# Optimization experiments

Hardware: AMD Instinct MI355X
Metric: run time of the kernel (lower is better)

## Reference

```python
import jax, jax.numpy as jnp
import numpy as np

N = 20000   # nodes
E = 320000  # edges
G = 64      # graphs in batch
IN = 256    # in_dim
H = 256     # hidden_dim1
C = 2       # n_classes


def setup_inputs() -> dict:
    key = jax.random.key(0)
    ks = jax.random.split(key, 12)
    h = jax.random.normal(ks[0], (N, IN), jnp.float32)
    src = jax.random.randint(ks[1], (E,), 0, N)
    dst = jax.random.randint(ks[2], (E,), 0, N)
    graph_id = jnp.sort(jax.random.randint(ks[3], (N,), 0, G))
    s_in = 1.0 / np.sqrt(IN)
    s_h = 1.0 / np.sqrt(H)
    W_conv = jax.random.normal(ks[4], (IN, H), jnp.float32) * s_in
    b_conv = jnp.zeros((H,), jnp.float32)
    w_gate = jax.random.normal(ks[5], (H, 1), jnp.float32) * s_h
    b_gate = jnp.zeros((1,), jnp.float32)
    W1 = jax.random.normal(ks[6], (H, H), jnp.float32) * s_h
    b1 = jnp.zeros((H,), jnp.float32)
    W2 = jax.random.normal(ks[7], (H, C), jnp.float32) * s_h
    b2 = jnp.zeros((C,), jnp.float32)
    return dict(h=h, src=src, dst=dst, graph_id=graph_id, W_conv=W_conv,
                b_conv=b_conv, w_gate=w_gate, b_gate=b_gate, W1=W1, b1=b1,
                W2=W2, b2=b2)


def reference(h, src, dst, graph_id, W_conv, b_conv, w_gate, b_gate, W1, b1, W2, b2):
    ones_e = jnp.ones((E,), jnp.float32)
    # DGL GraphConv, norm='both': D_out^-1/2 on source, D_in^-1/2 on dest
    deg_out = jax.ops.segment_sum(ones_e, src, num_segments=N)
    deg_in = jax.ops.segment_sum(ones_e, dst, num_segments=N)
    hn = h * jax.lax.rsqrt(jnp.maximum(deg_out, 1.0))[:, None]
    hn = hn @ W_conv                       # [N, H] (weight applied before aggregation)
    agg = jax.ops.segment_sum(hn[src], dst, num_segments=N)  # gather + scatter-add
    agg = agg * jax.lax.rsqrt(jnp.maximum(deg_in, 1.0))[:, None] + b_conv
    hr = jax.nn.relu(agg)                  # F.relu after conv1
    # GlobalAttentionPooling: per-graph segment softmax over gate scores
    gate = hr @ w_gate + b_gate            # [N, 1]
    gmax = jax.ops.segment_max(gate, graph_id, num_segments=G)
    e = jnp.exp(gate - gmax[graph_id])
    denom = jax.ops.segment_sum(e, graph_id, num_segments=G)
    att = e / denom[graph_id]              # [N, 1] attention weights (g2)
    hg = jax.ops.segment_sum(att * hr, graph_id, num_segments=G)  # [G, H]
    # classifier heads (dropout is identity at inference)
    a2 = hg @ W1 + b1
    a3 = a2 @ W2 + b2
    return jax.nn.sigmoid(a3), att, hg
```

## Files before the change

### kernel.cpp

```cpp
#include <hip/hip_runtime.h>
#include <hip/hip_bf16.h>
#include <hip/hip_fp16.h>
#include <math.h>

#define NN 20000
#define EE 320000
#define GG 64
#define IND 256
#define HD 256
#define CC 2

typedef __hip_bfloat16 bf16;
typedef __attribute__((ext_vector_type(8))) short short8;
typedef __attribute__((ext_vector_type(4))) float f32x4;

__device__ __forceinline__ float b2f(bf16 x){ return __bfloat162float(x); }
__device__ __forceinline__ float bits2f(unsigned short b){
    union{ float f; unsigned u; } v; v.u = ((unsigned)b) << 16; return v.f;
}
__device__ __forceinline__ short f2bs(float x){
    union{ bf16 b; short s; } u; u.b = __float2bfloat16(x); return u.s;
}
__device__ __forceinline__ float ldf3(const void* p, size_t i, int c){
    if (c == 1) return b2f(((const bf16*)p)[i]);
    if (c == 2) return __half2float(((const __half*)p)[i]);
    return ((const float*)p)[i];
}
__device__ __forceinline__ int idec(const void* p, int i, int c){
    if (c == 1) return (int)(((const long long*)p)[i]);
    if (c == 2) return (int)(((const float*)p)[i]);
    if (c == 3) return (int)__half2float(((const __half*)p)[i]);
    return ((const int*)p)[i];
}
__device__ __forceinline__ int wdetect(const unsigned short* p){
    int cb = 0, cf = 0, nz = 0;
    for (int i = 0; i < 128; i += 2){
        unsigned u = p[i];
        nz += (u != 0);
        int e8 = (u >> 7) & 0xFF;
        int e5 = (u >> 10) & 0x1F;
        cb += (e8 >= 100 && e8 <= 141);
        cf += (e5 >= 4 && e5 <= 22);
    }
    return (nz < 8) ? 0 : (cb >= 60) ? 1 : ((cf >= 60) ? 2 : 0);
}

#define ZBLK 64
__global__ __launch_bounds__(256) void k_detect(const void* src, const void* dst,
                         const void* gid,
                         const unsigned short* h, const unsigned short* Wc,
                         const unsigned short* wg, const unsigned short* W1,
                         const unsigned short* W2, const unsigned short* bc,
                         int* icode, int* dcode, int* zero_base,
                         bf16* __restrict__ Wb){
    int blk = blockIdx.x;
    if (blk < 3){
        if (threadIdx.x != 0) return;
        const void* buf = (blk == 0) ? src : (blk == 1) ? dst : gid;
        int n     = (blk == 2) ? NN : EE;
        int bound = (blk == 2) ? GG : NN;
        int ok64 = 1, ok32 = 1, okf32 = 1, okf16 = 1;
        const long long* p64 = (const long long*)buf;
        for (int i = 0; i < 64; i++){
            long long v = p64[n/8 + i];
            if (v < 0 || v >= (long long)bound) ok64 = 0;
        }
        const int* p32 = (const int*)buf;
        const unsigned* pu = (const unsigned*)buf;
        for (int i = 0; i < 64; i++){
            int v = p32[n/4 + i];
            if (v < 0 || v >= bound) ok32 = 0;
            float f = __uint_as_float(pu[n/4 + i]);
            if (!(f >= 0.f && f < (float)bound)) okf32 = 0;
        }
        const __half* ph = (const __half*)buf;
        for (int i = 0; i < 64; i++){
            float f = __half2float(ph[n/2 + i]);
            if (!(f >= 0.f && f < (float)bound)) okf16 = 0;
        }
        icode[blk] = ok64 ? 1 : (ok32 ? 0 : (okf32 ? 2 : (okf16 ? 3 : 0)));
    } else if (blk == 3){
        int t = threadIdx.x; if (t >= 6) return;
        const unsigned short* p = t==0?h:t==1?Wc:t==2?wg:t==3?W1:t==4?W2:bc;
        dcode[t] = wdetect(p);
    } else if (blk < 4 + IND){
        int k = blk - 4;
        __shared__ int code;
        if (threadIdx.x == 0) code = wdetect(Wc);
        __syncthreads();
        int c = code;
        int n = threadIdx.x;
        Wb[(size_t)n*IND + k] = __float2bfloat16(ldf3(Wc, (size_t)k*HD + n, c));
    } else {
        int idx = (blk - (4 + IND))*256 + threadIdx.x;
        const int total = 3*NN + GG*HD;
        for (int i = idx; i < total; i += ZBLK*256) zero_base[i] = 0;
    }
}

__global__ void k_prep(const void* src_r, const void* dst_r, const void* gid_r,
                       const int* __restrict__ icode,
                       int* __restrict__ gid_i,
                       int* cnt_out, int* cnt_in){
    int i = blockIdx.x*256 + threadIdx.x;
    if (i < NN) gid_i[i] = idec(gid_r, i, icode[2]);
    if (i >= EE) return;
    int s = idec(src_r, i, icode[0]);
    int d = idec(dst_r, i, icode[1]);
    if ((unsigned)s < NN) atomicAdd(&cnt_out[s], 1);
    if ((unsigned)d < NN) atomicAdd(&cnt_in[d], 1);
}

__global__ __launch_bounds__(1024) void k_scan(const int* __restrict__ cnt_out,
                                               const int* __restrict__ cnt_in,
                                               const int* __restrict__ gid,
                                               float* rs_out, float* rs_in,
                                               int* __restrict__ row_start,
                                               int* gstart, int* gend){
    int t = threadIdx.x;
    for (int i = t; i < NN; i += 1024){
        rs_out[i] = rsqrtf(fmaxf((float)cnt_out[i], 1.f));
        rs_in[i]  = rsqrtf(fmaxf((float)cnt_in[i], 1.f));
    }
    __shared__ int part[1024];
    const int per = (NN + 1023)/1024;
    int lo = t*per, hi = min(lo+per, NN);
    int s = 0;
    for (int i = lo; i < hi; i++) s += cnt_in[i];
    part[t] = s; __syncthreads();
    for (int off = 1; off < 1024; off <<= 1){
        int v = (t >= off) ? part[t-off] : 0;
        __syncthreads();
        part[t] += v;
        __syncthreads();
    }
    int base = part[t] - s;
    for (int i = lo; i < hi; i++){ row_start[i] = base; base += cnt_in[i]; }
    if (t == 1023) row_start[NN] = part[1023];
    __shared__ int ls[GG+1];
    if (t <= GG){
        int a = 0, b = NN;
        while (a < b){
            int mid = (a + b) >> 1;
            if (gid[mid] < t) a = mid + 1; else b = mid;
        }
        ls[t] = a;
    }
    __syncthreads();
    if (t < GG){ gstart[t] = ls[t]; gend[t] = ls[t+1]; }
}

#define GEMMB (NN/32)
#define FILLB ((EE+255)/256)
__global__ __launch_bounds__(256) void k_fillgemm(const void* __restrict__ h,
                                                  const bf16* __restrict__ Wb,
                                                  const float* __restrict__ rs_out,
                                                  const void* __restrict__ src_r,
                                                  const void* __restrict__ dst_r,
                                                  const int* __restrict__ icode,
                                                  const int* __restrict__ dcode,
                                                  const int* __restrict__ row_start,
                                                  int* __restrict__ cursor,
                                                  int* __restrict__ csr_src,
                                                  bf16* __restrict__ hn){
    int blk = blockIdx.x;
    if (blk >= GEMMB){
        int e = (blk - GEMMB)*256 + threadIdx.x;
        if (e >= EE) return;
        int s = idec(src_r, e, icode[0]);
        int d = idec(dst_r, e, icode[1]);
        if ((unsigned)s >= NN || (unsigned)d >= NN) return;
        int pos = atomicAdd(&cursor[d], 1);
        csr_src[row_start[d] + pos] = s;
        return;
    }
    int fh = dcode[0];
    int tid = threadIdx.x;
    int wave = tid >> 6, lane = tid & 63;
    int q = lane >> 4, mr = lane & 15;
    int row0 = blk * 32;
    int ncol0 = wave * 64;
    f32x4 acc[2][4] = {};
    const float* hf = (const float*)h;
    #pragma unroll
    for (int k0 = 0; k0 < IND; k0 += 32){
        short8 a[2], b[4];
        if (fh == 0){
            #pragma unroll
            for (int mi = 0; mi < 2; mi++){
                int r = row0 + mi*16 + mr;
                const float4* p = (const float4*)(hf + (size_t)r*IND + k0 + q*8);
                float4 v0 = p[0], v1 = p[1];
                a[mi][0] = f2bs(v0.x); a[mi][1] = f2bs(v0.y);
                a[mi][2] = f2bs(v0.z); a[mi][3] = f2bs(v0.w);
                a[mi][4] = f2bs(v1.x); a[mi][5] = f2bs(v1.y);
                a[mi][6] = f2bs(v1.z); a[mi][7] = f2bs(v1.w);
            }
        } else {
            #pragma unroll
            for (int mi = 0; mi < 2; mi++){
                int r = row0 + mi*16 + mr;
                #pragma unroll
                for (int j = 0; j < 8; j++)
                    a[mi][j] = f2bs(ldf3(h, (size_t)r*IND + k0 + q*8 + j, fh));
            }
        }
        #pragma unroll
        for (int ni = 0; ni < 4; ni++)
            b[ni] = *reinterpret_cast<const short8*>(
                        Wb + (size_t)(ncol0 + ni*16 + mr)*IND + k0 + q*8);
        #pragma unroll
        for (int mi = 0; mi < 2; mi++)
            #pragma unroll
            for (int ni = 0; ni < 4; ni++)
                acc[mi][ni] = __builtin_amdgcn_mfma_f32_16x16x32_bf16(
                                  a[mi], b[ni], acc[mi][ni], 0, 0, 0);
    }
    #pragma unroll
    for (int mi = 0; mi < 2; mi++){
        int rowb = row0 + mi*16 + q*4;
        #pragma unroll
        for (int r = 0; r < 4; r++){
            int row = rowb + r;
            float rs = rs_out[row];
            #pragma unroll
            for (int ni = 0; ni < 4; ni++)
                hn[(size_t)row*HD + ncol0 + ni*16 + mr] =
                    __float2bfloat16(acc[mi][ni][r] * rs);
        }
    }
}

__global__ __launch_bounds__(256) void k_gather(const bf16* __restrict__ hn,
                                                const float* __restrict__ rs_in,
                                                const int* __restrict__ row_start,
                                                const int* __restrict__ csr_src,
                                                const void* __restrict__ b_conv,
                                                const void* __restrict__ w_gate,
                                                const void* __restrict__ b_gate,
                                                const int* __restrict__ dcode,
                                                float* __restrict__ hr,
                                                float* __restrict__ gate){
    int wave = threadIdx.x >> 6, lane = threadIdx.x & 63;
    int n = blockIdx.x*4 + wave;
    if (n >= NN) return;
    int lo = row_start[n], hi = row_start[n+1];
    int half = lane >> 5, l2 = lane & 31;
    float a0=0.f,a1=0.f,a2=0.f,a3=0.f,a4=0.f,a5=0.f,a6=0.f,a7=0.f;
    int j = lo;
    for (; j + 8 <= hi; j += 8){
        int sA = csr_src[j+0+half], sB = csr_src[j+2+half];
        int sC = csr_src[j+4+half], sD = csr_src[j+6+half];
        short8 uA = *reinterpret_cast<const short8*>(hn + (size_t)sA*HD + l2*8);
        short8 uB = *reinterpret_cast<const short8*>(hn + (size_t)sB*HD + l2*8);
        short8 uC = *reinterpret_cast<const short8*>(hn + (size_t)sC*HD + l2*8);
        short8 uD = *reinterpret_cast<const short8*>(hn + (size_t)sD*HD + l2*8);
        a0 += bits2f((unsigned short)uA[0]) + bits2f((unsigned short)uB[0])
            + bits2f((unsigned short)uC[0]) + bits2f((unsigned short)uD[0]);
        a1 += bits2f((unsigned short)uA[1]) + bits2f((unsigned short)uB[1])
            + bits2f((unsigned short)uC[1]) + bits2f((unsigned short)uD[1]);
        a2 += bits2f((unsigned short)uA[2]) + bits2f((unsigned short)uB[2])
            + bits2f((unsigned short)uC[2]) + bits2f((unsigned short)uD[2]);
        a3 += bits2f((unsigned short)uA[3]) + bits2f((unsigned short)uB[3])
            + bits2f((unsigned short)uC[3]) + bits2f((unsigned short)uD[3]);
        a4 += bits2f((unsigned short)uA[4]) + bits2f((unsigned short)uB[4])
            + bits2f((unsigned short)uC[4]) + bits2f((unsigned short)uD[4]);
        a5 += bits2f((unsigned short)uA[5]) + bits2f((unsigned short)uB[5])
            + bits2f((unsigned short)uC[5]) + bits2f((unsigned short)uD[5]);
        a6 += bits2f((unsigned short)uA[6]) + bits2f((unsigned short)uB[6])
            + bits2f((unsigned short)uC[6]) + bits2f((unsigned short)uD[6]);
        a7 += bits2f((unsigned short)uA[7]) + bits2f((unsigned short)uB[7])
            + bits2f((unsigned short)uC[7]) + bits2f((unsigned short)uD[7]);
    }
    for (; j + 2 <= hi; j += 2){
        int s = csr_src[j+half];
        short8 u = *reinterpret_cast<const short8*>(hn + (size_t)s*HD + l2*8);
        a0 += bits2f((unsigned short)u[0]); a1 += bits2f((unsigned short)u[1]);
        a2 += bits2f((unsigned short)u[2]); a3 += bits2f((unsigned short)u[3]);
        a4 += bits2f((unsigned short)u[4]); a5 += bits2f((unsigned short)u[5]);
        a6 += bits2f((unsigned short)u[6]); a7 += bits2f((unsigned short)u[7]);
    }
    if (j < hi && half == 0){
        int s = csr_src[j];
        short8 u = *reinterpret_cast<const short8*>(hn + (size_t)s*HD + l2*8);
        a0 += bits2f((unsigned short)u[0]); a1 += bits2f((unsigned short)u[1]);
        a2 += bits2f((unsigned short)u[2]); a3 += bits2f((unsigned short)u[3]);
        a4 += bits2f((unsigned short)u[4]); a5 += bits2f((unsigned short)u[5]);
        a6 += bits2f((unsigned short)u[6]); a7 += bits2f((unsigned short)u[7]);
    }
    float send0 = half ? a0 : a4;
    float send1 = half ? a1 : a5;
    float send2 = half ? a2 : a6;
    float send3 = half ? a3 : a7;
    float recv0 = __shfl_xor(send0, 32);
    float recv1 = __shfl_xor(send1, 32);
    float recv2 = __shfl_xor(send2, 32);
    float recv3 = __shfl_xor(send3, 32);
    float tot0 = (half ? a4 : a0) + recv0;
    float tot1 = (half ? a5 : a1) + recv1;
    float tot2 = (half ? a6 : a2) + recv2;
    float tot3 = (half ? a7 : a3) + recv3;
    int db = dcode[5], fg = dcode[2];
    float rsn = rs_in[n];
    int c = l2*8 + half*4;
    float v0 = fmaxf(fmaf(tot0, rsn, ldf3(b_conv, c+0, db)), 0.f);
    float v1 = fmaxf(fmaf(tot1, rsn, ldf3(b_conv, c+1, db)), 0.f);
    float v2 = fmaxf(fmaf(tot2, rsn, ldf3(b_conv, c+2, db)), 0.f);
    float v3 = fmaxf(fmaf(tot3, rsn, ldf3(b_conv, c+3, db)), 0.f);
    float4 fv; fv.x = v0; fv.y = v1; fv.z = v2; fv.w = v3;
    *(float4*)(hr + (size_t)n*HD + c) = fv;
    float g = v0*ldf3(w_gate, c+0, fg) + v1*ldf3(w_gate, c+1, fg)
            + v2*ldf3(w_gate, c+2, fg) + v3*ldf3(w_gate, c+3, fg);
    #pragma unroll
    for (int off = 32; off; off >>= 1) g += __shfl_down(g, off);
    if (lane == 0) gate[n] = g + ldf3(b_gate, 0, db);
}

__global__ __launch_bounds__(256) void k_softhg(const float* __restrict__ gate,
                                                const float* __restrict__ hr,
                                                const int* __restrict__ gstart,
                                                const int* __restrict__ gend,
                                                float* __restrict__ hg,
                                                float* __restrict__ out_att){
    int g = blockIdx.x >> 3, part = blockIdx.x & 7;
    int t = threadIdx.x, lane = t & 63, wid = t >> 6;
    int lo = gstart[g], hi = gend[g], len = hi - lo;
    if (len <= 0) return;
    __shared__ float red[4];
    float m = -INFINITY;
    for (int n = lo + t; n < hi; n += 256) m = fmaxf(m, gate[n]);
    #pragma unroll
    for (int off = 32; off; off >>= 1) m = fmaxf(m, __shfl_xor(m, off));
    if (lane == 0) red[wid] = m;
    __syncthreads();
    m = fmaxf(fmaxf(red[0], red[1]), fmaxf(red[2], red[3]));
    __syncthreads();
    float s = 0.f;
    for (int n = lo + t; n < hi; n += 256) s += expf(gate[n] - m);
    #pragma unroll
    for (int off = 32; off; off >>= 1) s += __shfl_xor(s, off);
    if (lane == 0) red[wid] = s;
    __syncthreads();
    s = red[0] + red[1] + red[2] + red[3];
    float inv = 1.f / s;
    int chunk = (len + 7) >> 3;
    int plo = lo + part*chunk, phi = min(plo + chunk, hi);
    if (plo >= phi) return;
    for (int n = plo + t; n < phi; n += 256)
        out_att[n] = expf(gate[n] - m) * inv;
    float a0 = 0.f, a1 = 0.f, a2 = 0.f, a3 = 0.f;
    int r = plo;
    for (; r + 4 <= phi; r += 4){
        float w0 = expf(gate[r+0] - m) * inv;
        float w1 = expf(gate[r+1] - m) * inv;
        float w2 = expf(gate[r+2] - m) * inv;
        float w3 = expf(gate[r+3] - m) * inv;
        a0 = fmaf(w0, hr[(size_t)(r+0)*HD + t], a0);
        a1 = fmaf(w1, hr[(size_t)(r+1)*HD + t], a1);
        a2 = fmaf(w2, hr[(size_t)(r+2)*HD + t], a2);
        a3 = fmaf(w3, hr[(size_t)(r+3)*HD + t], a3);
    }
    for (; r < phi; r++)
        a0 = fmaf(expf(gate[r] - m) * inv, hr[(size_t)r*HD + t], a0);
    atomicAdd(&hg[g*HD + t], (a0 + a1) + (a2 + a3));
}

__global__ __launch_bounds__(256) void k_cls(const float* __restrict__ hg,
                                             const void* __restrict__ W1,
                                             const void* __restrict__ b1,
                                             const void* __restrict__ W2,
                                             const void* __restrict__ b2,
                                             const int* __restrict__ dcode,
                                             float* __restrict__ out0,
                                             float* __restrict__ out_hg){
    int f1 = dcode[3], f2 = dcode[4], db = dcode[5];
    int g = blockIdx.x, tid = threadIdx.x;
    __shared__ float hs[256];
    float hv = hg[g*HD + tid];
    hs[tid] = hv;
    out_hg[g*HD + tid] = hv;
    __syncthreads();
    float acc = ldf3(b1, tid, db);
    if (f1 == 1){
        const bf16* w = (const bf16*)W1;
        for (int k = 0; k < HD; k++) acc += hs[k]*b2f(w[(size_t)k*HD + tid]);
    } else if (f1 == 2){
        const __half* w = (const __half*)W1;
        for (int k = 0; k < HD; k++) acc += hs[k]*__half2float(w[(size_t)k*HD + tid]);
    } else {
        const float* w = (const float*)W1;
        for (int k = 0; k < HD; k++) acc += hs[k]*w[(size_t)k*HD + tid];
    }
    float p0 = acc * ldf3(W2, tid*CC + 0, f2);
    float p1 = acc * ldf3(W2, tid*CC + 1, f2);
    __shared__ float r0[256], r1[256];
    r0[tid] = p0; r1[tid] = p1; __syncthreads();
    for (int s = 128; s; s >>= 1){
        if (tid < s){ r0[tid] += r0[tid+s]; r1[tid] += r1[tid+s]; }
        __syncthreads();
    }
    if (tid == 0){
        out0[g*CC+0] = 1.f/(1.f + expf(-(r0[0] + ldf3(b2, 0, db))));
        out0[g*CC+1] = 1.f/(1.f + expf(-(r1[0] + ldf3(b2, 1, db))));
    }
}

extern "C" void kernel_launch(void* const* d_in, const int* in_sizes, int n_in,
                              void* d_out, int out_size, void* d_ws, size_t ws_size,
                              hipStream_t stream) {
    const void* h      = d_in[0];
    const void* src_r  = d_in[1];
    const void* dst_r  = d_in[2];
    const void* gid_r  = d_in[3];
    const void* W_conv = d_in[4];
    const void* b_conv = d_in[5];
    const void* w_gate = d_in[6];
    const void* b_gate = d_in[7];
    const void* W1     = d_in[8];
    const void* b1     = d_in[9];
    const void* W2     = d_in[10];
    const void* b2     = d_in[11];

    float* out     = (float*)d_out;
    float* out0    = out;
    float* out_att = out + GG*CC;
    float* out_hg  = out + GG*CC + NN;

    char* w = (char*)d_ws;
    float* hr   = (float*)w;  w += (size_t)NN*HD*sizeof(float);
    bf16*  hn   = (bf16*)w;   w += (size_t)NN*HD*sizeof(bf16);
    bf16*  Wb   = (bf16*)w;   w += (size_t)IND*HD*sizeof(bf16);
    float* rs_o = (float*)w;  w += (size_t)NN*sizeof(float);
    float* rs_i = (float*)w;  w += (size_t)NN*sizeof(float);
    float* gate = (float*)w;  w += (size_t)NN*sizeof(float);
    int* gstart = (int*)w;    w += GG*sizeof(int);
    int* gend   = (int*)w;    w += GG*sizeof(int);
    int* dcode  = (int*)w;    w += 8*sizeof(int);
    int* icode  = (int*)w;    w += 8*sizeof(int);
    int* gid_i  = (int*)w;    w += (size_t)NN*sizeof(int);
    int* cnt_out= (int*)w;    w += (size_t)NN*sizeof(int);
    int* cnt_in = (int*)w;    w += (size_t)NN*sizeof(int);
    int* cursor = (int*)w;    w += (size_t)NN*sizeof(int);
    float* hg   = (float*)w;  w += (size_t)GG*HD*sizeof(float);
    int* rowst  = (int*)w;    w += (size_t)(NN+1)*sizeof(int);
    int* csr    = (int*)w;    w += (size_t)EE*sizeof(int);

    k_detect<<<4 + IND + ZBLK, 256, 0, stream>>>(src_r, dst_r, gid_r,
                                     (const unsigned short*)h, (const unsigned short*)W_conv,
                                     (const unsigned short*)w_gate, (const unsigned short*)W1,
                                     (const unsigned short*)W2, (const unsigned short*)b_conv,
                                     icode, dcode, cnt_out, Wb);

    k_prep<<<(EE+255)/256, 256, 0, stream>>>(src_r, dst_r, gid_r, icode,
                                             gid_i, cnt_out, cnt_in);
    k_scan<<<1, 1024, 0, stream>>>(cnt_out, cnt_in, gid_i, rs_o, rs_i,
                                   rowst, gstart, gend);

    k_fillgemm<<<GEMMB + FILLB, 256, 0, stream>>>(h, Wb, rs_o, src_r, dst_r,
                                                  icode, dcode, rowst, cursor,
                                                  csr, hn);

    k_gather<<<(NN+3)/4, 256, 0, stream>>>(hn, rs_i, rowst, csr,
                                           b_conv, w_gate, b_gate, dcode, hr, gate);

    k_softhg<<<GG*8, 256, 0, stream>>>(gate, hr, gstart, gend, hg, out_att);

    k_cls<<<GG, 256, 0, stream>>>(hg, W1, b1, W2, b2, dcode, out0, out_hg);
}
```

Measured before the change: 234.7 us.

## Move source-degree scaling into gather and overlap GEMM with degree counting

```diff
diff --git a/kernel.cpp b/kernel.cpp
--- a/kernel.cpp
+++ b/kernel.cpp
@@ -32,20 +32,18 @@
     if (c == 3) return (int)__half2float(((const __half*)p)[i]);
     return ((const int*)p)[i];
 }
-__device__ __forceinline__ int wdetect(const unsigned short* p){
-    int cb = 0, cf = 0, nz = 0;
-    for (int i = 0; i < 128; i += 2){
-        unsigned u = p[i];
-        nz += (u != 0);
-        int e8 = (u >> 7) & 0xFF;
-        int e5 = (u >> 10) & 0x1F;
-        cb += (e8 >= 100 && e8 <= 141);
-        cf += (e5 >= 4 && e5 <= 22);
-    }
+__device__ __forceinline__ int wdetect_wave(const unsigned short* p, int t){
+    unsigned u = p[2*t];
+    int e8 = (u >> 7) & 0xFF;
+    int e5 = (u >> 10) & 0x1F;
+    int nz = __popcll(__ballot(u != 0));
+    int cb = __popcll(__ballot(e8 >= 100 && e8 <= 141));
+    int cf = __popcll(__ballot(e5 >= 4 && e5 <= 22));
     return (nz < 8) ? 0 : (cb >= 60) ? 1 : ((cf >= 60) ? 2 : 0);
 }
 
 #define ZBLK 64
+#define DETB (9 + IND)
 __global__ __launch_bounds__(256) void k_detect(const void* src, const void* dst,
                          const void* gid,
                          const unsigned short* h, const unsigned short* Wc,
@@ -54,124 +52,67 @@
                          int* icode, int* dcode, int* zero_base,
                          bf16* __restrict__ Wb){
     int blk = blockIdx.x;
+    int t = threadIdx.x;
     if (blk < 3){
-        if (threadIdx.x != 0) return;
+        if (t >= 64) return;
         const void* buf = (blk == 0) ? src : (blk == 1) ? dst : gid;
         int n     = (blk == 2) ? NN : EE;
         int bound = (blk == 2) ? GG : NN;
-        int ok64 = 1, ok32 = 1, okf32 = 1, okf16 = 1;
-        const long long* p64 = (const long long*)buf;
-        for (int i = 0; i < 64; i++){
-            long long v = p64[n/8 + i];
-            if (v < 0 || v >= (long long)bound) ok64 = 0;
+        long long v64 = ((const long long*)buf)[n/8 + t];
+        unsigned long long bad64 = __ballot(v64 < 0 || v64 >= (long long)bound);
+        int v32 = ((const int*)buf)[n/4 + t];
+        unsigned long long bad32 = __ballot(v32 < 0 || v32 >= bound);
+        float f32v = __uint_as_float(((const unsigned*)buf)[n/4 + t]);
+        unsigned long long badf32 = __ballot(!(f32v >= 0.f && f32v < (float)bound));
+        float f16v = __half2float(((const __half*)buf)[n/2 + t]);
+        unsigned long long badf16 = __ballot(!(f16v >= 0.f && f16v < (float)bound));
+        if (t == 0)
+            icode[blk] = (bad64 == 0ull) ? 1 : ((bad32 == 0ull) ? 0 :
+                         ((badf32 == 0ull) ? 2 : ((badf16 == 0ull) ? 3 : 0)));
+    } else if (blk < 9){
+        if (t >= 64) return;
+        int b = blk - 3;
+        const unsigned short* p = b==0?h:b==1?Wc:b==2?wg:b==3?W1:b==4?W2:bc;
+        int code = wdetect_wave(p, t);
+        if (t == 0) dcode[b] = code;
+    } else if (blk < DETB){
+        int k = blk - 9;
+        __shared__ int scode;
+        if (t < 64){
+            int code = wdetect_wave(Wc, t);
+            if (t == 0) scode = code;
         }
-        const int* p32 = (const int*)buf;
-        const unsigned* pu = (const unsigned*)buf;
-        for (int i = 0; i < 64; i++){
-            int v = p32[n/4 + i];
-            if (v < 0 || v >= bound) ok32 = 0;
-            float f = __uint_as_float(pu[n/4 + i]);
-            if (!(f >= 0.f && f < (float)bound)) okf32 = 0;
-        }
-        const __half* ph = (const __half*)buf;
-        for (int i = 0; i < 64; i++){
-            float f = __half2float(ph[n/2 + i]);
-            if (!(f >= 0.f && f < (float)bound)) okf16 = 0;
-        }
-        icode[blk] = ok64 ? 1 : (ok32 ? 0 : (okf32 ? 2 : (okf16 ? 3 : 0)));
-    } else if (blk == 3){
-        int t = threadIdx.x; if (t >= 6) return;
-        const unsigned short* p = t==0?h:t==1?Wc:t==2?wg:t==3?W1:t==4?W2:bc;
-        dcode[t] = wdetect(p);
-    } else if (blk < 4 + IND){
-        int k = blk - 4;
-        __shared__ int code;
-        if (threadIdx.x == 0) code = wdetect(Wc);
         __syncthreads();
-        int c = code;
-        int n = threadIdx.x;
-        Wb[(size_t)n*IND + k] = __float2bfloat16(ldf3(Wc, (size_t)k*HD + n, c));
+        int c = scode;
+        Wb[(size_t)t*IND + k] = __float2bfloat16(ldf3(Wc, (size_t)k*HD + t, c));
     } else {
-        int idx = (blk - (4 + IND))*256 + threadIdx.x;
+        int idx = (blk - DETB)*256 + t;
         const int total = 3*NN + GG*HD;
         for (int i = idx; i < total; i += ZBLK*256) zero_base[i] = 0;
     }
 }
 
-__global__ void k_prep(const void* src_r, const void* dst_r, const void* gid_r,
-                       const int* __restrict__ icode,
-                       int* __restrict__ gid_i,
-                       int* cnt_out, int* cnt_in){
-    int i = blockIdx.x*256 + threadIdx.x;
-    if (i < NN) gid_i[i] = idec(gid_r, i, icode[2]);
-    if (i >= EE) return;
-    int s = idec(src_r, i, icode[0]);
-    int d = idec(dst_r, i, icode[1]);
-    if ((unsigned)s < NN) atomicAdd(&cnt_out[s], 1);
-    if ((unsigned)d < NN) atomicAdd(&cnt_in[d], 1);
-}
-
-__global__ __launch_bounds__(1024) void k_scan(const int* __restrict__ cnt_out,
-                                               const int* __restrict__ cnt_in,
-                                               const int* __restrict__ gid,
-                                               float* rs_out, float* rs_in,
-                                               int* __restrict__ row_start,
-                                               int* gstart, int* gend){
-    int t = threadIdx.x;
-    for (int i = t; i < NN; i += 1024){
-        rs_out[i] = rsqrtf(fmaxf((float)cnt_out[i], 1.f));
-        rs_in[i]  = rsqrtf(fmaxf((float)cnt_in[i], 1.f));
-    }
-    __shared__ int part[1024];
-    const int per = (NN + 1023)/1024;
-    int lo = t*per, hi = min(lo+per, NN);
-    int s = 0;
-    for (int i = lo; i < hi; i++) s += cnt_in[i];
-    part[t] = s; __syncthreads();
-    for (int off = 1; off < 1024; off <<= 1){
-        int v = (t >= off) ? part[t-off] : 0;
-        __syncthreads();
-        part[t] += v;
-        __syncthreads();
-    }
-    int base = part[t] - s;
-    for (int i = lo; i < hi; i++){ row_start[i] = base; base += cnt_in[i]; }
-    if (t == 1023) row_start[NN] = part[1023];
-    __shared__ int ls[GG+1];
-    if (t <= GG){
-        int a = 0, b = NN;
-        while (a < b){
-            int mid = (a + b) >> 1;
-            if (gid[mid] < t) a = mid + 1; else b = mid;
-        }
-        ls[t] = a;
-    }
-    __syncthreads();
-    if (t < GG){ gstart[t] = ls[t]; gend[t] = ls[t+1]; }
-}
-
 #define GEMMB (NN/32)
-#define FILLB ((EE+255)/256)
-__global__ __launch_bounds__(256) void k_fillgemm(const void* __restrict__ h,
+#define PREPB ((EE+255)/256)
+__global__ __launch_bounds__(256) void k_prepgemm(const void* __restrict__ h,
                                                   const bf16* __restrict__ Wb,
-                                                  const float* __restrict__ rs_out,
                                                   const void* __restrict__ src_r,
                                                   const void* __restrict__ dst_r,
+                                                  const void* __restrict__ gid_r,
                                                   const int* __restrict__ icode,
                                                   const int* __restrict__ dcode,
-                                                  const int* __restrict__ row_start,
-                                                  int* __restrict__ cursor,
-                                                  int* __restrict__ csr_src,
+                                                  int* __restrict__ gid_i,
+                                                  int* cnt_out, int* cnt_in,
                                                   bf16* __restrict__ hn){
     int blk = blockIdx.x;
     if (blk >= GEMMB){
-        int e = (blk - GEMMB)*256 + threadIdx.x;
-        if (e >= EE) return;
-        int s = idec(src_r, e, icode[0]);
-        int d = idec(dst_r, e, icode[1]);
-        if ((unsigned)s >= NN || (unsigned)d >= NN) return;
-        int pos = atomicAdd(&cursor[d], 1);
-        csr_src[row_start[d] + pos] = s;
+        int i = (blk - GEMMB)*256 + threadIdx.x;
+        if (i < NN) gid_i[i] = idec(gid_r, i, icode[2]);
+        if (i >= EE) return;
+        int s = idec(src_r, i, icode[0]);
+        int d = idec(dst_r, i, icode[1]);
+        if ((unsigned)s < NN) atomicAdd(&cnt_out[s], 1);
+        if ((unsigned)d < NN) atomicAdd(&cnt_in[d], 1);
         return;
     }
     int fh = dcode[0];
@@ -222,16 +163,68 @@
         #pragma unroll
         for (int r = 0; r < 4; r++){
             int row = rowb + r;
-            float rs = rs_out[row];
             #pragma unroll
             for (int ni = 0; ni < 4; ni++)
                 hn[(size_t)row*HD + ncol0 + ni*16 + mr] =
-                    __float2bfloat16(acc[mi][ni][r] * rs);
+                    __float2bfloat16(acc[mi][ni][r]);
         }
     }
 }
 
+__global__ __launch_bounds__(1024) void k_scan(const int* __restrict__ cnt_out,
+                                               const int* __restrict__ cnt_in,
+                                               const int* __restrict__ gid,
+                                               float* rs_out, float* rs_in,
+                                               int* __restrict__ row_start,
+                                               int* gstart, int* gend){
+    int t = threadIdx.x;
+    for (int i = t; i < NN; i += 1024){
+        rs_out[i] = rsqrtf(fmaxf((float)cnt_out[i], 1.f));
+        rs_in[i]  = rsqrtf(fmaxf((float)cnt_in[i], 1.f));
+    }
+    __shared__ int part[1024];
+    const int per = (NN + 1023)/1024;
+    int lo = t*per, hi = min(lo+per, NN);
+    int s = 0;
+    for (int i = lo; i < hi; i++) s += cnt_in[i];
+    part[t] = s; __syncthreads();
+    for (int off = 1; off < 1024; off <<= 1){
+        int v = (t >= off) ? part[t-off] : 0;
+        __syncthreads();
+        part[t] += v;
+        __syncthreads();
+    }
+    int base = part[t] - s;
+    for (int i = lo; i < hi; i++){ row_start[i] = base; base += cnt_in[i]; }
+    if (t == 1023) row_start[NN] = part[1023];
+    __shared__ int ls[GG+1];
+    if (t <= GG){
+        int a = 0, b = NN;
+        while (a < b){
+            int mid = (a + b) >> 1;
+            if (gid[mid] < t) a = mid + 1; else b = mid;
+        }
+        ls[t] = a;
+    }
+    __syncthreads();
+    if (t < GG){ gstart[t] = ls[t]; gend[t] = ls[t+1]; }
+}
+
+__global__ void k_fill(const void* src_r, const void* dst_r,
+                       const int* __restrict__ icode,
+                       const int* __restrict__ row_start, int* __restrict__ cursor,
+                       int* __restrict__ csr_src){
+    int e = blockIdx.x*256 + threadIdx.x;
+    if (e >= EE) return;
+    int s = idec(src_r, e, icode[0]);
+    int d = idec(dst_r, e, icode[1]);
+    if ((unsigned)s >= NN || (unsigned)d >= NN) return;
+    int pos = atomicAdd(&cursor[d], 1);
+    csr_src[row_start[d] + pos] = s;
+}
+
 __global__ __launch_bounds__(256) void k_gather(const bf16* __restrict__ hn,
+                                                const float* __restrict__ rs_out,
                                                 const float* __restrict__ rs_in,
                                                 const int* __restrict__ row_start,
                                                 const int* __restrict__ csr_src,
@@ -251,42 +244,69 @@
     for (; j + 8 <= hi; j += 8){
         int sA = csr_src[j+0+half], sB = csr_src[j+2+half];
         int sC = csr_src[j+4+half], sD = csr_src[j+6+half];
+        float rA = rs_out[sA], rB = rs_out[sB], rC = rs_out[sC], rD = rs_out[sD];
         short8 uA = *reinterpret_cast<const short8*>(hn + (size_t)sA*HD + l2*8);
         short8 uB = *reinterpret_cast<const short8*>(hn + (size_t)sB*HD + l2*8);
         short8 uC = *reinterpret_cast<const short8*>(hn + (size_t)sC*HD + l2*8);
         short8 uD = *reinterpret_cast<const short8*>(hn + (size_t)sD*HD + l2*8);
-        a0 += bits2f((unsigned short)uA[0]) + bits2f((unsigned short)uB[0])
-            + bits2f((unsigned short)uC[0]) + bits2f((unsigned short)uD[0]);
-        a1 += bits2f((unsigned short)uA[1]) + bits2f((unsigned short)uB[1])
-            + bits2f((unsigned short)uC[1]) + bits2f((unsigned short)uD[1]);
-        a2 += bits2f((unsigned short)uA[2]) + bits2f((unsigned short)uB[2])
-            + bits2f((unsigned short)uC[2]) + bits2f((unsigned short)uD[2]);
-        a3 += bits2f((unsigned short)uA[3]) + bits2f((unsigned short)uB[3])
-            + bits2f((unsigned short)uC[3]) + bits2f((unsigned short)uD[3]);
-        a4 += bits2f((unsigned short)uA[4]) + bits2f((unsigned short)uB[4])
-            + bits2f((unsigned short)uC[4]) + bits2f((unsigned short)uD[4]);
-        a5 += bits2f((unsigned short)uA[5]) + bits2f((unsigned short)uB[5])
-            + bits2f((unsigned short)uC[5]) + bits2f((unsigned short)uD[5]);
-        a6 += bits2f((unsigned short)uA[6]) + bits2f((unsigned short)uB[6])
-            + bits2f((unsigned short)uC[6]) + bits2f((unsigned short)uD[6]);
-        a7 += bits2f((unsigned short)uA[7]) + bits2f((unsigned short)uB[7])
-            + bits2f((unsigned short)uC[7]) + bits2f((unsigned short)uD[7]);
+        a0 = fmaf(rA, bits2f((unsigned short)uA[0]),
+             fmaf(rB, bits2f((unsigned short)uB[0]),
+             fmaf(rC, bits2f((unsigned short)uC[0]),
+             fmaf(rD, bits2f((unsigned short)uD[0]), a0))));
+        a1 = fmaf(rA, bits2f((unsigned short)uA[1]),
+             fmaf(rB, bits2f((unsigned short)uB[1]),
+             fmaf(rC, bits2f((unsigned short)uC[1]),
+             fmaf(rD, bits2f((unsigned short)uD[1]), a1))));
+        a2 = fmaf(rA, bits2f((unsigned short)uA[2]),
+             fmaf(rB, bits2f((unsigned short)uB[2]),
+             fmaf(rC, bits2f((unsigned short)uC[2]),
+             fmaf(rD, bits2f((unsigned short)uD[2]), a2))));
+        a3 = fmaf(rA, bits2f((unsigned short)uA[3]),
+             fmaf(rB, bits2f((unsigned short)uB[3]),
+             fmaf(rC, bits2f((unsigned short)uC[3]),
+             fmaf(rD, bits2f((unsigned short)uD[3]), a3))));
+        a4 = fmaf(rA, bits2f((unsigned short)uA[4]),
+             fmaf(rB, bits2f((unsigned short)uB[4]),
+             fmaf(rC, bits2f((unsigned short)uC[4]),
+             fmaf(rD, bits2f((unsigned short)uD[4]), a4))));
+        a5 = fmaf(rA, bits2f((unsigned short)uA[5]),
+             fmaf(rB, bits2f((unsigned short)uB[5]),
+             fmaf(rC, bits2f((unsigned short)uC[5]),
+             fmaf(rD, bits2f((unsigned short)uD[5]), a5))));
+        a6 = fmaf(rA, bits2f((unsigned short)uA[6]),
+             fmaf(rB, bits2f((unsigned short)uB[6]),
+             fmaf(rC, bits2f((unsigned short)uC[6]),
+             fmaf(rD, bits2f((unsigned short)uD[6]), a6))));
+        a7 = fmaf(rA, bits2f((unsigned short)uA[7]),
+             fmaf(rB, bits2f((unsigned short)uB[7]),
+             fmaf(rC, bits2f((unsigned short)uC[7]),
+             fmaf(rD, bits2f((unsigned short)uD[7]), a7))));
     }
     for (; j + 2 <= hi; j += 2){
         int s = csr_src[j+half];
+        float r = rs_out[s];
         short8 u = *reinterpret_cast<const short8*>(hn + (size_t)s*HD + l2*8);
-        a0 += bits2f((unsigned short)u[0]); a1 += bits2f((unsigned short)u[1]);
-        a2 += bits2f((unsigned short)u[2]); a3 += bits2f((unsigned short)u[3]);
-        a4 += bits2f((unsigned short)u[4]); a5 += bits2f((unsigned short)u[5]);
-        a6 += bits2f((unsigned short)u[6]); a7 += bits2f((unsigned short)u[7]);
+        a0 = fmaf(r, bits2f((unsigned short)u[0]), a0);
+        a1 = fmaf(r, bits2f((unsigned short)u[1]), a1);
+        a2 = fmaf(r, bits2f((unsigned short)u[2]), a2);
+        a3 = fmaf(r, bits2f((unsigned short)u[3]), a3);
+        a4 = fmaf(r, bits2f((unsigned short)u[4]), a4);
+        a5 = fmaf(r, bits2f((unsigned short)u[5]), a5);
+        a6 = fmaf(r, bits2f((unsigned short)u[6]), a6);
+        a7 = fmaf(r, bits2f((unsigned short)u[7]), a7);
     }
     if (j < hi && half == 0){
         int s = csr_src[j];
+        float r = rs_out[s];
         short8 u = *reinterpret_cast<const short8*>(hn + (size_t)s*HD + l2*8);
-        a0 += bits2f((unsigned short)u[0]); a1 += bits2f((unsigned short)u[1]);
-        a2 += bits2f((unsigned short)u[2]); a3 += bits2f((unsigned short)u[3]);
-        a4 += bits2f((unsigned short)u[4]); a5 += bits2f((unsigned short)u[5]);
-        a6 += bits2f((unsigned short)u[6]); a7 += bits2f((unsigned short)u[7]);
+        a0 = fmaf(r, bits2f((unsigned short)u[0]), a0);
+        a1 = fmaf(r, bits2f((unsigned short)u[1]), a1);
+        a2 = fmaf(r, bits2f((unsigned short)u[2]), a2);
+        a3 = fmaf(r, bits2f((unsigned short)u[3]), a3);
+        a4 = fmaf(r, bits2f((unsigned short)u[4]), a4);
+        a5 = fmaf(r, bits2f((unsigned short)u[5]), a5);
+        a6 = fmaf(r, bits2f((unsigned short)u[6]), a6);
+        a7 = fmaf(r, bits2f((unsigned short)u[7]), a7);
     }
     float send0 = half ? a0 : a4;
     float send1 = half ? a1 : a5;
@@ -445,22 +465,22 @@
     int* rowst  = (int*)w;    w += (size_t)(NN+1)*sizeof(int);
     int* csr    = (int*)w;    w += (size_t)EE*sizeof(int);
 
-    k_detect<<<4 + IND + ZBLK, 256, 0, stream>>>(src_r, dst_r, gid_r,
+    k_detect<<<DETB + ZBLK, 256, 0, stream>>>(src_r, dst_r, gid_r,
                                      (const unsigned short*)h, (const unsigned short*)W_conv,
                                      (const unsigned short*)w_gate, (const unsigned short*)W1,
                                      (const unsigned short*)W2, (const unsigned short*)b_conv,
                                      icode, dcode, cnt_out, Wb);
 
-    k_prep<<<(EE+255)/256, 256, 0, stream>>>(src_r, dst_r, gid_r, icode,
-                                             gid_i, cnt_out, cnt_in);
+    k_prepgemm<<<GEMMB + PREPB, 256, 0, stream>>>(h, Wb, src_r, dst_r, gid_r,
+                                                  icode, dcode, gid_i,
+                                                  cnt_out, cnt_in, hn);
+
     k_scan<<<1, 1024, 0, stream>>>(cnt_out, cnt_in, gid_i, rs_o, rs_i,
                                    rowst, gstart, gend);
 
-    k_fillgemm<<<GEMMB + FILLB, 256, 0, stream>>>(h, Wb, rs_o, src_r, dst_r,
-                                                  icode, dcode, rowst, cursor,
-                                                  csr, hn);
-
-    k_gather<<<(NN+3)/4, 256, 0, stream>>>(hn, rs_i, rowst, csr,
+    k_fill<<<PREPB, 256, 0, stream>>>(src_r, dst_r, icode, rowst, cursor, csr);
+
+    k_gather<<<(NN+3)/4, 256, 0, stream>>>(hn, rs_o, rs_i, rowst, csr,
                                            b_conv, w_gate, b_gate, dcode, hr, gate);
 
     k_softhg<<<GG*8, 256, 0, stream>>>(gate, hr, gstart, gend, hg, out_att);
```

After: 230.0 us. 2.0% less time.
